# Performance work log

Measured on AMD Instinct MI355X. Metric: run time of the kernel, lower is better.

The kernel has to match this reference:

```python
import jax, jax.numpy as jnp
import numpy as np

N, E = 50000, 800000
HID, HEADS, EDIM = 64, 4, 32
HC = HID * HEADS
NEG_SLOPE = 0.2
LN_EPS = 1e-5


def setup_inputs() -> dict:
    key = jax.random.key(0)
    ks = jax.random.split(key, 16)
    s = lambda d: 1.0 / np.sqrt(d)
    return {
        "x": jax.random.normal(ks[0], (N, HID), jnp.float32),
        "edge_index": jax.random.randint(ks[1], (2, E), 0, N, jnp.int64),
        "edge_attr": jax.random.normal(ks[2], (E, EDIM), jnp.float32),
        # GATv2Conv params
        "W_l": jax.random.normal(ks[3], (HID, HC), jnp.float32) * s(HID),
        "b_l": jnp.zeros((HC,), jnp.float32),
        "W_r": jax.random.normal(ks[4], (HID, HC), jnp.float32) * s(HID),
        "b_r": jnp.zeros((HC,), jnp.float32),
        "W_e": jax.random.normal(ks[5], (EDIM, HC), jnp.float32) * s(EDIM),
        "att": jax.random.normal(ks[6], (HEADS, HID), jnp.float32) * s(HID),
        "bias_gat": jnp.zeros((HC,), jnp.float32),
        # block params
        "W1": jax.random.normal(ks[7], (HID, HC), jnp.float32) * s(HID),
        "b1": jnp.zeros((HC,), jnp.float32),
        "gamma": jnp.ones((HC,), jnp.float32),
        "beta": jnp.zeros((HC,), jnp.float32),
        "W2": jax.random.normal(ks[8], (HC, HID), jnp.float32) * s(HC),
        "b2": jnp.zeros((HID,), jnp.float32),
    }


def _gatv2(x, edge_index, edge_attr, W_l, b_l, W_r, b_r, W_e, att, bias_gat):
    src, dst = edge_index[0], edge_index[1]
    x_l = (x @ W_l + b_l).reshape(N, HEADS, HID)  # source transform
    x_r = (x @ W_r + b_r).reshape(N, HEADS, HID)  # target transform
    e = (edge_attr @ W_e).reshape(E, HEADS, HID)
    m = x_l[src] + x_r[dst] + e                    # [E, H, C]
    m = jax.nn.leaky_relu(m, NEG_SLOPE)
    alpha = jnp.einsum('ehc,hc->eh', m, att)       # [E, H]
    # segment softmax over incoming edges of each target node
    amax = jax.ops.segment_max(alpha, dst, num_segments=N)
    alpha = jnp.exp(alpha - amax[dst])
    denom = jax.ops.segment_sum(alpha, dst, num_segments=N)
    alpha = alpha / (denom[dst] + 1e-16)
    out = jax.ops.segment_sum(x_l[src] * alpha[..., None], dst, num_segments=N)
    return out.reshape(N, HC) + bias_gat


def reference(x, edge_index, edge_attr, W_l, b_l, W_r, b_r, W_e, att, bias_gat,
              W1, b1, gamma, beta, W2, b2):
    h = _gatv2(x, edge_index, edge_attr, W_l, b_l, W_r, b_r, W_e, att, bias_gat)
    xl = jnp.tanh(x @ W1 + b1)
    z = xl + h
    mu = jnp.mean(z, axis=-1, keepdims=True)
    var = jnp.var(z, axis=-1, keepdims=True)
    z = (z - mu) * jax.lax.rsqrt(var + LN_EPS) * gamma + beta
    return jnp.tanh(z @ W2 + b2)
```

## Files before the change

### kernel.cpp

```cpp
#include <hip/hip_runtime.h>
#include <math.h>

#define N_NODES 50000
#define N_EDGES 800000
#define HID 64
#define HEADS 4
#define HC 256
#define NEG_SLOPE 0.2f
#define LN_EPS 1e-5f
#define EDGE_BLOCKS 2048

typedef __attribute__((ext_vector_type(8))) short bf16x8;
typedef __attribute__((ext_vector_type(8))) unsigned short u16x8;
typedef __attribute__((ext_vector_type(4))) float f32x4;

__device__ __forceinline__ float bf2f(unsigned short u) {
    return __uint_as_float(((unsigned int)u) << 16);
}
__device__ __forceinline__ unsigned short f2bf(float f) {
    unsigned int u = __float_as_uint(f);
    u = (u + 0x7fffu + ((u >> 16) & 1u)) >> 16;
    return (unsigned short)u;
}
__device__ __forceinline__ float fast_tanh(float v) {
    const float c = fminf(fmaxf(v, -15.f), 15.f);
    const float e = __expf(2.f * c);
    return 1.f - 2.f / (e + 1.f);
}
__device__ __forceinline__ bf16x8 pack_bf8(float4 a, float4 b) {
    u16x8 r;
    r[0] = f2bf(a.x); r[1] = f2bf(a.y); r[2] = f2bf(a.z); r[3] = f2bf(a.w);
    r[4] = f2bf(b.x); r[5] = f2bf(b.y); r[6] = f2bf(b.z); r[7] = f2bf(b.w);
    return __builtin_bit_cast(bf16x8, r);
}

__global__ __launch_bounds__(256) void k_ntm(
    const float* __restrict__ x,
    const float* __restrict__ W_l, const float* __restrict__ b_l,
    const float* __restrict__ W_r, const float* __restrict__ b_r,
    unsigned short* __restrict__ xl_t, unsigned short* __restrict__ xr_t)
{
    __shared__ unsigned short wl_s[2][16][64][8];
    __shared__ unsigned short wr_s[2][16][64][8];
    const int t = threadIdx.x, lane = t & 63, wv = t >> 6;
    const int arow = lane & 15, koct = lane >> 4;

    for (int i = t; i < 2048; i += 256) {
        const int ks = i >> 10, nt = (i >> 6) & 15, ls = i & 63;
        const int col = nt * 16 + (ls & 15);
        const int kb = ks * 32 + (ls >> 4) * 8;
        unsigned short a[8], b[8];
#pragma unroll
        for (int j = 0; j < 8; j++) {
            a[j] = f2bf(W_l[(kb + j) * 256 + col]);
            b[j] = f2bf(W_r[(kb + j) * 256 + col]);
        }
        *(ushort4*)&wl_s[ks][nt][ls][0] = make_ushort4(a[0], a[1], a[2], a[3]);
        *(ushort4*)&wl_s[ks][nt][ls][4] = make_ushort4(a[4], a[5], a[6], a[7]);
        *(ushort4*)&wr_s[ks][nt][ls][0] = make_ushort4(b[0], b[1], b[2], b[3]);
        *(ushort4*)&wr_s[ks][nt][ls][4] = make_ushort4(b[4], b[5], b[6], b[7]);
    }
    __syncthreads();

    const int n0w = blockIdx.x * 64 + wv * 16;
    if (n0w >= N_NODES) return;

    const float* xrow = x + (size_t)(n0w + arow) * 64;
    const bf16x8 af0 = pack_bf8(*(const float4*)(xrow + koct * 8),
                                *(const float4*)(xrow + koct * 8 + 4));
    const bf16x8 af1 = pack_bf8(*(const float4*)(xrow + 32 + koct * 8),
                                *(const float4*)(xrow + 32 + koct * 8 + 4));

    float acc[4][16];
#pragma unroll
    for (int nt = 0; nt < 16; nt++) {
        const float bv = b_l[nt * 16 + arow];
        f32x4 d = {bv, bv, bv, bv};
        d = __builtin_amdgcn_mfma_f32_16x16x32_bf16(af0, *(const bf16x8*)&wl_s[0][nt][lane][0], d, 0, 0, 0);
        d = __builtin_amdgcn_mfma_f32_16x16x32_bf16(af1, *(const bf16x8*)&wl_s[1][nt][lane][0], d, 0, 0, 0);
#pragma unroll
        for (int r = 0; r < 4; r++) acc[r][nt] = d[r];
    }
#pragma unroll
    for (int r = 0; r < 4; r++) {
        u16x8 lo, hi;
#pragma unroll
        for (int j = 0; j < 8; j++) { lo[j] = f2bf(acc[r][j]); hi[j] = f2bf(acc[r][j + 8]); }
        unsigned short* dst = xl_t + (size_t)(n0w + koct * 4 + r) * 256 + arow * 16;
        *(u16x8*)dst = lo;
        *(u16x8*)(dst + 8) = hi;
    }
#pragma unroll
    for (int nt = 0; nt < 16; nt++) {
        const float bv = b_r[nt * 16 + arow];
        f32x4 d = {bv, bv, bv, bv};
        d = __builtin_amdgcn_mfma_f32_16x16x32_bf16(af0, *(const bf16x8*)&wr_s[0][nt][lane][0], d, 0, 0, 0);
        d = __builtin_amdgcn_mfma_f32_16x16x32_bf16(af1, *(const bf16x8*)&wr_s[1][nt][lane][0], d, 0, 0, 0);
#pragma unroll
        for (int r = 0; r < 4; r++) acc[r][nt] = d[r];
    }
#pragma unroll
    for (int r = 0; r < 4; r++) {
        u16x8 lo, hi;
#pragma unroll
        for (int j = 0; j < 8; j++) { lo[j] = f2bf(acc[r][j]); hi[j] = f2bf(acc[r][j + 8]); }
        unsigned short* dst = xr_t + (size_t)(n0w + koct * 4 + r) * 256 + arow * 16;
        *(u16x8*)dst = lo;
        *(u16x8*)(dst + 8) = hi;
    }
}

__global__ __launch_bounds__(256) void k_permw(
    const float* __restrict__ W1, const float* __restrict__ b1,
    const float* __restrict__ gamma, const float* __restrict__ beta,
    const float* __restrict__ bias_gat, const float* __restrict__ W2,
    float* __restrict__ W1p, float* __restrict__ b1p,
    float* __restrict__ gammap, float* __restrict__ betap,
    float* __restrict__ biasgp, float* __restrict__ W2p)
{
    const int c = threadIdx.x;
    const int pos = (c & 15) * 16 + (c >> 4);
    for (int k = 0; k < 64; k++) W1p[k * 256 + pos] = W1[k * 256 + c];
    b1p[pos] = b1[c];
    gammap[pos] = gamma[c];
    betap[pos] = beta[c];
    biasgp[pos] = bias_gat[c];
    for (int j = 0; j < 64; j++) W2p[pos * 64 + j] = W2[c * 64 + j];
}

__global__ __launch_bounds__(256) void k_hist(const int* __restrict__ ei, int* __restrict__ count)
{
    const int e = blockIdx.x * 256 + threadIdx.x;
    if (e < N_EDGES) atomicAdd(&count[ei[N_EDGES + e]], 1);
}

__global__ __launch_bounds__(1024) void k_scan(const int* __restrict__ count, int* __restrict__ off)
{
    __shared__ int wsum[16];
    __shared__ int s_carry;
    const int t = threadIdx.x, lane = t & 63, wv = t >> 6;
    if (t == 0) s_carry = 0;
    __syncthreads();
    for (int base = 0; base < N_NODES; base += 8192) {
        const int idx0 = base + t * 8;
        int v[8];
#pragma unroll
        for (int j = 0; j < 8; j++) { int i = idx0 + j; v[j] = (i < N_NODES) ? count[i] : 0; }
#pragma unroll
        for (int j = 1; j < 8; j++) v[j] += v[j - 1];
        const int tot = v[7];
        int sc = tot;
#pragma unroll
        for (int s = 1; s < 64; s <<= 1) { int o = __shfl_up(sc, s, 64); if (lane >= s) sc += o; }
        if (lane == 63) wsum[wv] = sc;
        __syncthreads();
        const int carry = s_carry;
        int woff = 0;
        for (int u = 0; u < wv; u++) woff += wsum[u];
        const int ebase = carry + woff + (sc - tot);
#pragma unroll
        for (int j = 0; j < 8; j++) {
            int i = idx0 + j;
            if (i < N_NODES) off[i] = ebase + (j ? v[j - 1] : 0);
        }
        __syncthreads();
        if (t == 0) { int tt = 0; for (int u = 0; u < 16; u++) tt += wsum[u]; s_carry = carry + tt; }
        __syncthreads();
    }
    if (threadIdx.x == 0) off[N_NODES] = s_carry;
}

__global__ __launch_bounds__(256) void k_scatter(
    const int* __restrict__ ei, const int* __restrict__ off, int* __restrict__ cursor,
    int* __restrict__ csr_src, int* __restrict__ eid_csr)
{
    const int e = blockIdx.x * 256 + threadIdx.x;
    if (e < N_EDGES) {
        const int s = ei[e];
        const int d = ei[N_EDGES + e];
        const int pos = off[d] + atomicAdd(&cursor[d], 1);
        csr_src[pos] = s;
        eid_csr[pos] = e;
    }
}

template<bool F32>
__global__ __launch_bounds__(256) void k_edgeagg(
    const int* __restrict__ off, const int* __restrict__ csr_src,
    const int* __restrict__ eid_csr, const float* __restrict__ edge_attr,
    const float* __restrict__ W_e, const float* __restrict__ att,
    const unsigned short* __restrict__ xl_t, const unsigned short* __restrict__ xr_t,
    void* __restrict__ zs_g)
{
    __shared__ unsigned short bfrag_s[16][64][8];

    const int t = threadIdx.x;
    const int lane = t & 63, wv = t >> 6;
    const int arow = lane & 15, koct = lane >> 4;

    for (int i = t; i < 1024; i += 256) {
        const int nt = i >> 6, ls = i & 63;
        const int col = nt * 16 + (ls & 15);
        const int kb = (ls >> 4) * 8;
        unsigned short tmp[8];
#pragma unroll
        for (int j = 0; j < 8; j++) tmp[j] = f2bf(W_e[(kb + j) * 256 + col]);
        *(ushort4*)&bfrag_s[nt][ls][0] = make_ushort4(tmp[0], tmp[1], tmp[2], tmp[3]);
        *(ushort4*)&bfrag_s[nt][ls][4] = make_ushort4(tmp[4], tmp[5], tmp[6], tmp[7]);
    }
    __syncthreads();

    float attLf[8], attHf[8];
#pragma unroll
    for (int j = 0; j < 8; j++) {
        attLf[j] = att[j * 16 + arow];
        attHf[j] = att[(j + 8) * 16 + arow];
    }

    const int STRIDE = EDGE_BLOCKS * 4;
    int node = blockIdx.x * 4 + wv;
    if (node >= N_NODES) return;

    int lo = off[node], hi = off[node + 1];
    u16x8 xrl = *(const u16x8*)(xr_t + (size_t)node * 256 + arow * 16);
    u16x8 xrh = *(const u16x8*)(xr_t + (size_t)node * 256 + arow * 16 + 8);
    while (hi <= lo) {
        if (F32) *(float4*)((float*)zs_g + (size_t)node * 256 + arow * 16 + koct * 4) = make_float4(0.f, 0.f, 0.f, 0.f);
        else *(ushort4*)((unsigned short*)zs_g + (size_t)node * 256 + arow * 16 + koct * 4) = make_ushort4(0, 0, 0, 0);
        node += STRIDE;
        if (node >= N_NODES) return;
        lo = off[node]; hi = off[node + 1];
        xrl = *(const u16x8*)(xr_t + (size_t)node * 256 + arow * 16);
        xrh = *(const u16x8*)(xr_t + (size_t)node * 256 + arow * 16 + 8);
    }
    int svbase = lo;
    int svall = csr_src[min(svbase + lane, hi - 1)];
    int evall = eid_csr[min(svbase + lane, hi - 1)];

    int nnode = node + STRIDE;
    bool nvalid = nnode < N_NODES;
    int nlo = 0, nhi = 0, nsvall = 0, nevall = 0;
    u16x8 nxrl = xrl, nxrh = xrh;
    if (nvalid) {
        nlo = off[nnode]; nhi = off[nnode + 1];
        nxrl = *(const u16x8*)(xr_t + (size_t)nnode * 256 + arow * 16);
        nxrh = *(const u16x8*)(xr_t + (size_t)nnode * 256 + arow * 16 + 8);
        if (nhi > nlo) {
            nsvall = csr_src[min(nlo + lane, nhi - 1)];
            nevall = eid_csr[min(nlo + lane, nhi - 1)];
        }
    }
    int p0 = lo;
    bf16x8 af;
    u16x8 xlo[4], xhi[4];
    {
        const int eid0 = __shfl(evall, arow, 64);
        const float* ap = edge_attr + (size_t)eid0 * 32 + koct * 8;
        af = pack_bf8(*(const float4*)ap, *(const float4*)(ap + 4));
#pragma unroll
        for (int r = 0; r < 4; r++) {
            const int sr = __shfl(svall, koct * 4 + r, 64);
            const unsigned short* bp = xl_t + (size_t)sr * 256 + arow * 16;
            xlo[r] = *(const u16x8*)bp;
            xhi[r] = *(const u16x8*)(bp + 8);
        }
    }

    float g[16];
#pragma unroll
    for (int i = 0; i < 16; i++) g[i] = 0.f;
    float dsum[4] = {0.f, 0.f, 0.f, 0.f};

    for (;;) {
        const bool last = (p0 + 16 >= hi);
        bool uvalid;
        int up0;
        if (!last) { uvalid = true; up0 = p0 + 16; }
        else {
            while (nvalid && nlo >= nhi) {
                if (F32) *(float4*)((float*)zs_g + (size_t)nnode * 256 + arow * 16 + koct * 4) = make_float4(0.f, 0.f, 0.f, 0.f);
                else *(ushort4*)((unsigned short*)zs_g + (size_t)nnode * 256 + arow * 16 + koct * 4) = make_ushort4(0, 0, 0, 0);
                nnode += STRIDE;
                nvalid = nnode < N_NODES;
                if (nvalid) {
                    nlo = off[nnode]; nhi = off[nnode + 1];
                    nxrl = *(const u16x8*)(xr_t + (size_t)nnode * 256 + arow * 16);
                    nxrh = *(const u16x8*)(xr_t + (size_t)nnode * 256 + arow * 16 + 8);
                    if (nhi > nlo) {
                        nsvall = csr_src[min(nlo + lane, nhi - 1)];
                        nevall = eid_csr[min(nlo + lane, nhi - 1)];
                    }
                }
            }
            uvalid = nvalid; up0 = nlo;
        }
        float4 uA0 = make_float4(0.f, 0.f, 0.f, 0.f), uA1 = uA0;
        if (uvalid) {
            const int ubase = last ? 0 : (up0 - svbase);
            const int uev = last ? nevall : evall;
            const int ueid = __shfl(uev, ubase + arow, 64);
            const float* ap = edge_attr + (size_t)ueid * 32 + koct * 8;
            uA0 = *(const float4*)ap;
            uA1 = *(const float4*)(ap + 4);
        }

        float s_[4][4];
#pragma unroll
        for (int r = 0; r < 4; r++)
#pragma unroll
            for (int h = 0; h < 4; h++) s_[r][h] = 0.f;

#pragma unroll
        for (int nt = 0; nt < 8; nt++) {
            const bf16x8 bfr = *(const bf16x8*)&bfrag_s[nt][lane][0];
            const float xrv = bf2f((unsigned short)xrl[nt]);
            f32x4 dacc = {xrv, xrv, xrv, xrv};
            dacc = __builtin_amdgcn_mfma_f32_16x16x32_bf16(af, bfr, dacc, 0, 0, 0);
            const float atv = attLf[nt];
            const int h = nt >> 2;
#pragma unroll
            for (int r = 0; r < 4; r++) {
                const float mm = dacc[r] + bf2f((unsigned short)xlo[r][nt]);
                const float lk = fmaxf(mm, NEG_SLOPE * mm);
                s_[r][h] = fmaf(atv, lk, s_[r][h]);
            }
        }
        u16x8 uxlo[4], uxhi[4];
        if (uvalid) {
            const int ubase = last ? 0 : (up0 - svbase);
            const int usrcv = last ? nsvall : svall;
#pragma unroll
            for (int r = 0; r < 4; r++) {
                const int sr = __shfl(usrcv, ubase + koct * 4 + r, 64);
                const unsigned short* bp = xl_t + (size_t)sr * 256 + arow * 16;
                uxlo[r] = *(const u16x8*)bp;
                uxhi[r] = *(const u16x8*)(bp + 8);
            }
        } else {
#pragma unroll
            for (int r = 0; r < 4; r++) { uxlo[r] = xlo[r]; uxhi[r] = xhi[r]; }
        }
#pragma unroll
        for (int n2 = 0; n2 < 8; n2++) {
            const int nt = n2 + 8;
            const bf16x8 bfr = *(const bf16x8*)&bfrag_s[nt][lane][0];
            const float xrv = bf2f((unsigned short)xrh[n2]);
            f32x4 dacc = {xrv, xrv, xrv, xrv};
            dacc = __builtin_amdgcn_mfma_f32_16x16x32_bf16(af, bfr, dacc, 0, 0, 0);
            const float atv = attHf[n2];
            const int h = nt >> 2;
#pragma unroll
            for (int r = 0; r < 4; r++) {
                const float mm = dacc[r] + bf2f((unsigned short)xhi[r][n2]);
                const float lk = fmaxf(mm, NEG_SLOPE * mm);
                s_[r][h] = fmaf(atv, lk, s_[r][h]);
            }
        }
#pragma unroll
        for (int r = 0; r < 4; r++)
#pragma unroll
            for (int h = 0; h < 4; h++) {
                float v = s_[r][h];
                v += __shfl_xor(v, 1, 64);
                v += __shfl_xor(v, 2, 64);
                v += __shfl_xor(v, 4, 64);
                v += __shfl_xor(v, 8, 64);
                s_[r][h] = v;
            }
#pragma unroll
        for (int h = 0; h < 4; h++) {
            float w4[4];
#pragma unroll
            for (int r = 0; r < 4; r++) {
                const bool ok = (p0 + koct * 4 + r) < hi;
                w4[r] = ok ? __expf(fminf(s_[r][h], 60.f)) : 0.f;
            }
            dsum[h] += (w4[0] + w4[1]) + (w4[2] + w4[3]);
#pragma unroll
            for (int q = 0; q < 4; q++) {
                const int nt = h * 4 + q;
                float acc = g[nt];
#pragma unroll
                for (int r = 0; r < 4; r++) {
                    const float xv = bf2f((unsigned short)(nt < 8 ? xlo[r][nt & 7] : xhi[r][nt & 7]));
                    acc = fmaf(w4[r], xv, acc);
                }
                g[nt] = acc;
            }
        }

        if (last) {
#pragma unroll
            for (int i = 0; i < 16; i++) {
                float v = g[i];
                v += __shfl_xor(v, 16, 64);
                v += __shfl_xor(v, 32, 64);
                g[i] = v;
            }
#pragma unroll
            for (int h = 0; h < 4; h++) {
                float v = dsum[h];
                v += __shfl_xor(v, 16, 64);
                v += __shfl_xor(v, 32, 64);
                dsum[h] = v;
            }
            const float inv = 1.f / (dsum[koct] + 1e-16f);
            if (F32) {
                *(float4*)((float*)zs_g + (size_t)node * 256 + arow * 16 + koct * 4) =
                    make_float4(g[koct * 4] * inv, g[koct * 4 + 1] * inv,
                                g[koct * 4 + 2] * inv, g[koct * 4 + 3] * inv);
            } else {
                *(ushort4*)((unsigned short*)zs_g + (size_t)node * 256 + arow * 16 + koct * 4) =
                    make_ushort4(f2bf(g[koct * 4] * inv), f2bf(g[koct * 4 + 1] * inv),
                                 f2bf(g[koct * 4 + 2] * inv), f2bf(g[koct * 4 + 3] * inv));
            }
            if (!uvalid) return;
            node = nnode; lo = nlo; hi = nhi; xrl = nxrl; xrh = nxrh;
            svbase = nlo; svall = nsvall; evall = nevall;
#pragma unroll
            for (int i = 0; i < 16; i++) g[i] = 0.f;
#pragma unroll
            for (int h = 0; h < 4; h++) dsum[h] = 0.f;
            nnode += STRIDE;
            nvalid = nnode < N_NODES;
            if (nvalid) {
                nlo = off[nnode]; nhi = off[nnode + 1];
                nxrl = *(const u16x8*)(xr_t + (size_t)nnode * 256 + arow * 16);
                nxrh = *(const u16x8*)(xr_t + (size_t)nnode * 256 + arow * 16 + 8);
                if (nhi > nlo) {
                    nsvall = csr_src[min(nlo + lane, nhi - 1)];
                    nevall = eid_csr[min(nlo + lane, nhi - 1)];
                }
            }
        }
        p0 = up0;
        af = pack_bf8(uA0, uA1);
#pragma unroll
        for (int r = 0; r < 4; r++) { xlo[r] = uxlo[r]; xhi[r] = uxhi[r]; }
        if (p0 - svbase >= 32) {
            svbase = p0;
            svall = csr_src[min(svbase + lane, hi - 1)];
            evall = eid_csr[min(svbase + lane, hi - 1)];
        }
    }
}

template<bool F32>
__global__ __launch_bounds__(256) void k_post(
    const void* __restrict__ zs_g, const float* __restrict__ x,
    const float* __restrict__ biasgp,
    const float* __restrict__ W1p, const float* __restrict__ b1p,
    const float* __restrict__ gammap, const float* __restrict__ betap,
    const float* __restrict__ W2p, const float* __restrict__ b2,
    float* __restrict__ out)
{
    __shared__ float xs[16][64];
    __shared__ float zsh[16][256];
    __shared__ float part[16][4][64];
    __shared__ float redS[16][4], redQ[16][4];

    const int n0 = blockIdx.x * 16;
    const int t = threadIdx.x, lane = t & 63, wv = t >> 6;

    for (int i = t; i < 16 * 64; i += 256) xs[i >> 6][i & 63] = x[n0 * 64 + i];
    __syncthreads();

    float a1[16];
    const float b1v = b1p[t];
#pragma unroll
    for (int n = 0; n < 16; n++) a1[n] = b1v;
    for (int k = 0; k < 64; k++) {
        const float w1v = W1p[k * 256 + t];
#pragma unroll
        for (int n = 0; n < 16; n++) a1[n] = fmaf(xs[n][k], w1v, a1[n]);
    }

    const float bg = biasgp[t];
    float z[16];
#pragma unroll
    for (int n = 0; n < 16; n++) {
        const float gv = F32 ? ((const float*)zs_g)[(size_t)(n0 + n) * 256 + t]
                             : bf2f(((const unsigned short*)zs_g)[(size_t)(n0 + n) * 256 + t]);
        z[n] = fast_tanh(a1[n]) + gv + bg;
    }

    const float gm = gammap[t], bt = betap[t];
#pragma unroll
    for (int n = 0; n < 16; n++) {
        float s = z[n], q = z[n] * z[n];
#pragma unroll
        for (int m = 1; m < 64; m <<= 1) { s += __shfl_xor(s, m, 64); q += __shfl_xor(q, m, 64); }
        if (lane == 0) { redS[n][wv] = s; redQ[n][wv] = q; }
    }
    __syncthreads();
#pragma unroll
    for (int n = 0; n < 16; n++) {
        const float s = redS[n][0] + redS[n][1] + redS[n][2] + redS[n][3];
        const float q = redQ[n][0] + redQ[n][1] + redQ[n][2] + redQ[n][3];
        const float mu = s * (1.f / 256.f);
        const float var = q * (1.f / 256.f) - mu * mu;
        const float ivn = rsqrtf(var + LN_EPS);
        zsh[n][t] = (z[n] - mu) * ivn * gm + bt;
    }
    __syncthreads();

    const int j = t & 63, qq = t >> 6;
    float p[16];
#pragma unroll
    for (int n = 0; n < 16; n++) p[n] = 0.f;
    for (int c0 = 0; c0 < 64; c0++) {
        const int c = qq * 64 + c0;
        const float w2v = W2p[c * 64 + j];
#pragma unroll
        for (int n = 0; n < 16; n++) p[n] = fmaf(zsh[n][c], w2v, p[n]);
    }
#pragma unroll
    for (int n = 0; n < 16; n++) part[n][qq][j] = p[n];
    __syncthreads();
#pragma unroll
    for (int i = 0; i < 4; i++) {
        const int n = wv * 4 + i;
        const float s = part[n][0][lane] + part[n][1][lane] + part[n][2][lane] + part[n][3][lane];
        out[(size_t)(n0 + n) * 64 + lane] = fast_tanh(s + b2[lane]);
    }
}

extern "C" void kernel_launch(void* const* d_in, const int* in_sizes, int n_in,
                              void* d_out, int out_size, void* d_ws, size_t ws_size,
                              hipStream_t stream)
{
    const float* x         = (const float*)d_in[0];
    const int*   ei        = (const int*)d_in[1];
    const float* edge_attr = (const float*)d_in[2];
    const float* W_l       = (const float*)d_in[3];
    const float* b_l       = (const float*)d_in[4];
    const float* W_r       = (const float*)d_in[5];
    const float* b_r       = (const float*)d_in[6];
    const float* W_e       = (const float*)d_in[7];
    const float* att       = (const float*)d_in[8];
    const float* bias_gat  = (const float*)d_in[9];
    const float* W1        = (const float*)d_in[10];
    const float* b1        = (const float*)d_in[11];
    const float* gamma     = (const float*)d_in[12];
    const float* beta      = (const float*)d_in[13];
    const float* W2        = (const float*)d_in[14];
    const float* b2        = (const float*)d_in[15];
    float* out = (float*)d_out;

    char* wsb = (char*)d_ws;
    size_t o = 0;
    unsigned short* xl_t   = (unsigned short*)(wsb + o);  o += (size_t)N_NODES * HC * 2;
    unsigned short* xr_t   = (unsigned short*)(wsb + o);  o += (size_t)N_NODES * HC * 2;
    int* csr_src           = (int*)(wsb + o);             o += (size_t)N_EDGES * 4;
    int* eid_csr           = (int*)(wsb + o);             o += (size_t)N_EDGES * 4;
    int* count             = (int*)(wsb + o);             o += (size_t)N_NODES * 4;
    int* cursor            = (int*)(wsb + o);             o += (size_t)N_NODES * 4;
    int* off               = (int*)(wsb + o);             o += (size_t)(N_NODES + 1) * 4;
    float* W1p             = (float*)(wsb + o);           o += 64 * 256 * 4;
    float* W2p             = (float*)(wsb + o);           o += 256 * 64 * 4;
    float* b1p             = (float*)(wsb + o);           o += 256 * 4;
    float* gammap          = (float*)(wsb + o);           o += 256 * 4;
    float* betap           = (float*)(wsb + o);           o += 256 * 4;
    float* biasgp          = (float*)(wsb + o);           o += 256 * 4;
    o = (o + 255) & ~(size_t)255;
    void* zs_g             = (void*)(wsb + o);
    const bool f32ok = (o + (size_t)N_NODES * HC * 4) <= ws_size;

    hipMemsetAsync(count, 0, 2 * (size_t)N_NODES * sizeof(int), stream);

    k_ntm<<<(N_NODES + 63) / 64, 256, 0, stream>>>(x, W_l, b_l, W_r, b_r, xl_t, xr_t);
    k_permw<<<1, 256, 0, stream>>>(W1, b1, gamma, beta, bias_gat, W2,
                                   W1p, b1p, gammap, betap, biasgp, W2p);
    k_hist<<<(N_EDGES + 255) / 256, 256, 0, stream>>>(ei, count);
    k_scan<<<1, 1024, 0, stream>>>(count, off);
    k_scatter<<<(N_EDGES + 255) / 256, 256, 0, stream>>>(ei, off, cursor, csr_src, eid_csr);
    if (f32ok) {
        k_edgeagg<true><<<EDGE_BLOCKS, 256, 0, stream>>>(off, csr_src, eid_csr, edge_attr,
                                                         W_e, att, xl_t, xr_t, zs_g);
        k_post<true><<<N_NODES / 16, 256, 0, stream>>>(zs_g, x, biasgp,
                                                       W1p, b1p, gammap, betap, W2p, b2, out);
    } else {
        k_edgeagg<false><<<EDGE_BLOCKS, 256, 0, stream>>>(off, csr_src, eid_csr, edge_attr,
                                                          W_e, att, xl_t, xr_t, zs_g);
        k_post<false><<<N_NODES / 16, 256, 0, stream>>>(zs_g, x, biasgp,
                                                        W1p, b1p, gammap, betap, W2p, b2, out);
    }
}
```

Measured before the change: 560.8 us.

## Rewrite post-processing kernel with bf16 MFMA matmuls over 64-node tiles

The node post-processing kernel now computes both dense projections (x@W1 and LayerNorm output @W2) with bf16 16x16x32 MFMA instructions instead of scalar FMA loops. Each block handles 64 nodes instead of 16, and weights are converted to bf16 fragment layout in shared memory once per block. LayerNorm reductions now run inside each wave's MFMA output layout, and results are staged through shared memory for coalesced stores. This lowers ALU cost, but it converts weights per block and uses bf16 operands, which reduces precision.

```diff
diff --git a/kernel.cpp b/kernel.cpp
--- a/kernel.cpp
+++ b/kernel.cpp
@@ -454,74 +454,124 @@
     const float* __restrict__ W2p, const float* __restrict__ b2,
     float* __restrict__ out)
 {
-    __shared__ float xs[16][64];
-    __shared__ float zsh[16][256];
-    __shared__ float part[16][4][64];
-    __shared__ float redS[16][4], redQ[16][4];
-
-    const int n0 = blockIdx.x * 16;
+    __shared__ unsigned short wf[16384];
+    __shared__ unsigned short zsh[64][272];
+    __shared__ float outsh[64][64];
+
     const int t = threadIdx.x, lane = t & 63, wv = t >> 6;
-
-    for (int i = t; i < 16 * 64; i += 256) xs[i >> 6][i & 63] = x[n0 * 64 + i];
+    const int arow = lane & 15, koct = lane >> 4;
+    const int n0 = blockIdx.x * 64;
+    const int nw = n0 + wv * 16;
+
+    for (int i = t; i < 2048; i += 256) {
+        const int ks = i >> 10, nt = (i >> 6) & 15, ls = i & 63;
+        const int col = (ls & 15) * 16 + nt;
+        const int kb = ks * 32 + (ls >> 4) * 8;
+        unsigned short a[8];
+#pragma unroll
+        for (int j = 0; j < 8; j++) a[j] = f2bf(W1p[(kb + j) * 256 + col]);
+        *(ushort4*)&wf[i * 8]     = make_ushort4(a[0], a[1], a[2], a[3]);
+        *(ushort4*)&wf[i * 8 + 4] = make_ushort4(a[4], a[5], a[6], a[7]);
+    }
     __syncthreads();
 
-    float a1[16];
-    const float b1v = b1p[t];
-#pragma unroll
-    for (int n = 0; n < 16; n++) a1[n] = b1v;
-    for (int k = 0; k < 64; k++) {
-        const float w1v = W1p[k * 256 + t];
-#pragma unroll
-        for (int n = 0; n < 16; n++) a1[n] = fmaf(xs[n][k], w1v, a1[n]);
-    }
-
-    const float bg = biasgp[t];
-    float z[16];
-#pragma unroll
-    for (int n = 0; n < 16; n++) {
-        const float gv = F32 ? ((const float*)zs_g)[(size_t)(n0 + n) * 256 + t]
-                             : bf2f(((const unsigned short*)zs_g)[(size_t)(n0 + n) * 256 + t]);
-        z[n] = fast_tanh(a1[n]) + gv + bg;
-    }
-
-    const float gm = gammap[t], bt = betap[t];
-#pragma unroll
-    for (int n = 0; n < 16; n++) {
-        float s = z[n], q = z[n] * z[n];
-#pragma unroll
-        for (int m = 1; m < 64; m <<= 1) { s += __shfl_xor(s, m, 64); q += __shfl_xor(q, m, 64); }
-        if (lane == 0) { redS[n][wv] = s; redQ[n][wv] = q; }
-    }
-    __syncthreads();
-#pragma unroll
-    for (int n = 0; n < 16; n++) {
-        const float s = redS[n][0] + redS[n][1] + redS[n][2] + redS[n][3];
-        const float q = redQ[n][0] + redQ[n][1] + redQ[n][2] + redQ[n][3];
+    const int xn = min(nw + arow, N_NODES - 1);
+    const float* xrow = x + (size_t)xn * 64;
+    const bf16x8 af0 = pack_bf8(*(const float4*)(xrow + koct * 8),
+                                *(const float4*)(xrow + koct * 8 + 4));
+    const bf16x8 af1 = pack_bf8(*(const float4*)(xrow + 32 + koct * 8),
+                                *(const float4*)(xrow + 32 + koct * 8 + 4));
+
+    float z[4][16];
+#pragma unroll
+    for (int nt = 0; nt < 16; nt++) {
+        const float bv = b1p[arow * 16 + nt];
+        f32x4 d = {bv, bv, bv, bv};
+        d = __builtin_amdgcn_mfma_f32_16x16x32_bf16(af0, *(const bf16x8*)&wf[(0 * 16 + nt) * 512 + lane * 8], d, 0, 0, 0);
+        d = __builtin_amdgcn_mfma_f32_16x16x32_bf16(af1, *(const bf16x8*)&wf[(1 * 16 + nt) * 512 + lane * 8], d, 0, 0, 0);
+#pragma unroll
+        for (int r = 0; r < 4; r++) z[r][nt] = d[r];
+    }
+#pragma unroll
+    for (int r = 0; r < 4; r++) {
+        const int nd = min(nw + koct * 4 + r, N_NODES - 1);
+        float gv[16];
+        if (F32) {
+            const float* gp = (const float*)zs_g + (size_t)nd * 256 + arow * 16;
+#pragma unroll
+            for (int i4 = 0; i4 < 4; i4++) {
+                const float4 v = *(const float4*)(gp + i4 * 4);
+                gv[i4 * 4] = v.x; gv[i4 * 4 + 1] = v.y; gv[i4 * 4 + 2] = v.z; gv[i4 * 4 + 3] = v.w;
+            }
+        } else {
+            const unsigned short* gp = (const unsigned short*)zs_g + (size_t)nd * 256 + arow * 16;
+            const u16x8 a = *(const u16x8*)gp;
+            const u16x8 b = *(const u16x8*)(gp + 8);
+#pragma unroll
+            for (int j = 0; j < 8; j++) { gv[j] = bf2f((unsigned short)a[j]); gv[j + 8] = bf2f((unsigned short)b[j]); }
+        }
+#pragma unroll
+        for (int nt = 0; nt < 16; nt++)
+            z[r][nt] = fast_tanh(z[r][nt]) + gv[nt] + biasgp[arow * 16 + nt];
+    }
+#pragma unroll
+    for (int r = 0; r < 4; r++) {
+        float s = 0.f, q = 0.f;
+#pragma unroll
+        for (int nt = 0; nt < 16; nt++) { s += z[r][nt]; q = fmaf(z[r][nt], z[r][nt], q); }
+        s += __shfl_xor(s, 1, 64); q += __shfl_xor(q, 1, 64);
+        s += __shfl_xor(s, 2, 64); q += __shfl_xor(q, 2, 64);
+        s += __shfl_xor(s, 4, 64); q += __shfl_xor(q, 4, 64);
+        s += __shfl_xor(s, 8, 64); q += __shfl_xor(q, 8, 64);
         const float mu = s * (1.f / 256.f);
         const float var = q * (1.f / 256.f) - mu * mu;
         const float ivn = rsqrtf(var + LN_EPS);
-        zsh[n][t] = (z[n] - mu) * ivn * gm + bt;
+        u16x8 lo, hi;
+#pragma unroll
+        for (int nt = 0; nt < 16; nt++) {
+            const float zn = (z[r][nt] - mu) * ivn * gammap[arow * 16 + nt] + betap[arow * 16 + nt];
+            if (nt < 8) lo[nt] = f2bf(zn); else hi[nt - 8] = f2bf(zn);
+        }
+        unsigned short* dst = &zsh[wv * 16 + koct * 4 + r][arow * 16];
+        *(u16x8*)dst = lo;
+        *(u16x8*)(dst + 8) = hi;
     }
     __syncthreads();
-
-    const int j = t & 63, qq = t >> 6;
-    float p[16];
-#pragma unroll
-    for (int n = 0; n < 16; n++) p[n] = 0.f;
-    for (int c0 = 0; c0 < 64; c0++) {
-        const int c = qq * 64 + c0;
-        const float w2v = W2p[c * 64 + j];
-#pragma unroll
-        for (int n = 0; n < 16; n++) p[n] = fmaf(zsh[n][c], w2v, p[n]);
-    }
-#pragma unroll
-    for (int n = 0; n < 16; n++) part[n][qq][j] = p[n];
+    for (int i = t; i < 2048; i += 256) {
+        const int kb = i >> 8, ct = (i >> 6) & 3, ls = i & 63;
+        const int col = ct * 16 + (ls & 15);
+        const int k0 = kb * 32 + (ls >> 4) * 8;
+        unsigned short a[8];
+#pragma unroll
+        for (int j = 0; j < 8; j++) a[j] = f2bf(W2p[(k0 + j) * 64 + col]);
+        *(ushort4*)&wf[i * 8]     = make_ushort4(a[0], a[1], a[2], a[3]);
+        *(ushort4*)&wf[i * 8 + 4] = make_ushort4(a[4], a[5], a[6], a[7]);
+    }
     __syncthreads();
-#pragma unroll
-    for (int i = 0; i < 4; i++) {
-        const int n = wv * 4 + i;
-        const float s = part[n][0][lane] + part[n][1][lane] + part[n][2][lane] + part[n][3][lane];
-        out[(size_t)(n0 + n) * 64 + lane] = fast_tanh(s + b2[lane]);
+    f32x4 acc2[4];
+#pragma unroll
+    for (int ct = 0; ct < 4; ct++) {
+        const float bv = b2[ct * 16 + arow];
+        acc2[ct][0] = bv; acc2[ct][1] = bv; acc2[ct][2] = bv; acc2[ct][3] = bv;
+    }
+#pragma unroll
+    for (int kb = 0; kb < 8; kb++) {
+        const bf16x8 a = *(const bf16x8*)&zsh[wv * 16 + arow][kb * 32 + koct * 8];
+#pragma unroll
+        for (int ct = 0; ct < 4; ct++)
+            acc2[ct] = __builtin_amdgcn_mfma_f32_16x16x32_bf16(
+                a, *(const bf16x8*)&wf[((kb * 4 + ct) * 64 + lane) * 8], acc2[ct], 0, 0, 0);
+    }
+#pragma unroll
+    for (int ct = 0; ct < 4; ct++)
+#pragma unroll
+        for (int r = 0; r < 4; r++)
+            outsh[wv * 16 + koct * 4 + r][ct * 16 + arow] = fast_tanh(acc2[ct][r]);
+    __syncthreads();
+    for (int i = t; i < 4096; i += 256) {
+        const int row = i >> 6;
+        if (n0 + row < N_NODES)
+            out[(size_t)(n0 + row) * 64 + (i & 63)] = outsh[row][i & 63];
     }
 }
 
@@ -577,12 +627,12 @@
     if (f32ok) {
         k_edgeagg<true><<<EDGE_BLOCKS, 256, 0, stream>>>(off, csr_src, eid_csr, edge_attr,
                                                          W_e, att, xl_t, xr_t, zs_g);
-        k_post<true><<<N_NODES / 16, 256, 0, stream>>>(zs_g, x, biasgp,
-                                                       W1p, b1p, gammap, betap, W2p, b2, out);
+        k_post<true><<<(N_NODES + 63) / 64, 256, 0, stream>>>(zs_g, x, biasgp,
+                                                              W1p, b1p, gammap, betap, W2p, b2, out);
     } else {
         k_edgeagg<false><<<EDGE_BLOCKS, 256, 0, stream>>>(off, csr_src, eid_csr, edge_attr,
                                                           W_e, att, xl_t, xr_t, zs_g);
-        k_post<false><<<N_NODES / 16, 256, 0, stream>>>(zs_g, x, biasgp,
-                                                        W1p, b1p, gammap, betap, W2p, b2, out);
-    }
-}
+        k_post<false><<<(N_NODES + 63) / 64, 256, 0, stream>>>(zs_g, x, biasgp,
+                                                               W1p, b1p, gammap, betap, W2p, b2, out);
+    }
+}
```

Result: faster. 528.3 us (-5.8%).
